# Kernel optimization log

Measured on AMD Instinct MI355X. Metric: run time of the kernel, lower is better.

Reference implementation:

```python
import jax, jax.numpy as jnp
import numpy as np
import math

N = 16384          # batch
F = 39             # field_size = len(feature_sizes)
V = 100000         # vocab per field
E = 16             # embedding_size
D = F * E          # d_model = 624
H = F              # heads = field_size
DK = D // H        # d_k = 16
L = 5              # len(hidden_dims) attention layers
OUT_DIM = 4
NUM_FFW = OUT_DIM * 3


def setup_inputs() -> dict:
    key = jax.random.key(0)
    ks = jax.random.split(key, 24)
    Xi = jax.random.randint(ks[0], (N, F, 1), 0, V, dtype=jnp.int64)
    Xv = jax.random.uniform(ks[1], (N, F), dtype=jnp.float32)
    # embedding tables (stacked across fields; all fields share vocab size)
    emb1 = jax.random.normal(ks[2], (F, V, 1), dtype=jnp.float32) * 0.02
    emb2 = jax.random.normal(ks[3], (F, V, E), dtype=jnp.float32) * 0.02
    # attention layer params, stacked over L layers; torch Linear stored as (in, out)
    s = 1.0 / math.sqrt(D)
    Wq = jax.random.normal(ks[4], (L, D, D), dtype=jnp.float32) * s
    Wk = jax.random.normal(ks[5], (L, D, D), dtype=jnp.float32) * s
    Wv = jax.random.normal(ks[6], (L, D, D), dtype=jnp.float32) * s
    Wo = jax.random.normal(ks[7], (L, D, D), dtype=jnp.float32) * s
    bq = jnp.zeros((L, D), dtype=jnp.float32)
    bk = jnp.zeros((L, D), dtype=jnp.float32)
    bv = jnp.zeros((L, D), dtype=jnp.float32)
    bo = jnp.zeros((L, D), dtype=jnp.float32)
    # merge linears: (F->4), (E->4), (D->4)
    m1_w = jax.random.normal(ks[8], (F, OUT_DIM), dtype=jnp.float32) / math.sqrt(F)
    m1_b = jnp.zeros((OUT_DIM,), dtype=jnp.float32)
    m2_w = jax.random.normal(ks[9], (E, OUT_DIM), dtype=jnp.float32) / math.sqrt(E)
    m2_b = jnp.zeros((OUT_DIM,), dtype=jnp.float32)
    m3_w = jax.random.normal(ks[10], (D, OUT_DIM), dtype=jnp.float32) / math.sqrt(D)
    m3_b = jnp.zeros((OUT_DIM,), dtype=jnp.float32)
    ffw_w = jax.random.normal(ks[11], (NUM_FFW, NUM_FFW), dtype=jnp.float32) / math.sqrt(NUM_FFW)
    ffw_b = jnp.zeros((NUM_FFW,), dtype=jnp.float32)
    # fm_dense_linear weight init'd to 1.0 in init_weight()
    fd_w = jnp.ones((NUM_FFW, 2), dtype=jnp.float32)
    fd_b = jnp.zeros((2,), dtype=jnp.float32)
    return dict(Xi=Xi, Xv=Xv, emb1=emb1, emb2=emb2,
                Wq=Wq, bq=bq, Wk=Wk, bk=bk, Wv=Wv, bv=bv, Wo=Wo, bo=bo,
                m1_w=m1_w, m1_b=m1_b, m2_w=m2_w, m2_b=m2_b, m3_w=m3_w, m3_b=m3_b,
                ffw_w=ffw_w, ffw_b=ffw_b, fd_w=fd_w, fd_b=fd_b)


def reference(Xi, Xv, emb1, emb2, Wq, bq, Wk, bk, Wv, bv, Wo, bo,
              m1_w, m1_b, m2_w, m2_b, m3_w, m3_b, ffw_w, ffw_b, fd_w, fd_b):
    idx = Xi[:, :, 0]                       # (N, F)
    far = jnp.arange(F)[None, :]            # (1, F) field index
    # --- FM first order: gather 1-d embeddings, scale by Xv ---
    f1 = emb1[far, idx][..., 0] * Xv        # (N, F)
    # --- FM second order: gather E-dim embeddings, scale, L2-normalize over fields ---
    xv = emb2[far, idx] * Xv[:, :, None]    # (N, F, E)
    norm = jnp.maximum(jnp.linalg.norm(xv, axis=1, keepdims=True), 1e-12)
    xv = xv / norm
    s1 = jnp.sum(xv, axis=1) ** 2           # (N, E)
    s2 = jnp.sum(xv ** 2, axis=1)           # (N, E)
    f2 = 0.5 * (s1 - s2)                    # (N, E)
    # --- deep part: stacked seq-len-1 multi-head attention ---
    x = xv.reshape(xv.shape[0], D)          # (N, D) deep_emb; deep_k = deep_q = x
    out = x
    inv_sqrt_dk = 1.0 / math.sqrt(DK)
    for l in range(L):
        # call is att(deep_k, deep_q, deep_out) -> forward(q=deep_k, k=deep_q, v=deep_out)
        q = (x @ Wq[l] + bq[l]).reshape(-1, H, DK)
        k = (x @ Wk[l] + bk[l]).reshape(-1, H, DK)
        v = (out @ Wv[l] + bv[l]).reshape(-1, H, DK)
        scores = jnp.sum(q * k, axis=-1, keepdims=True) * inv_sqrt_dk  # (N, H, 1)
        att = scores * v                                               # (N, H, DK)
        out = att.reshape(-1, D) @ Wo[l] + bo[l]
    # --- merge + head ---
    h1 = f1 @ m1_w + m1_b                   # (N, 4)
    h2 = f2 @ m2_w + m2_b                   # (N, 4)
    h3 = out @ m3_w + m3_b                  # (N, 4)
    ffw_in = jnp.concatenate([h1, h2, h3], axis=1)   # (N, 12)
    ffw_out = jax.nn.relu(ffw_in @ ffw_w + ffw_b)    # (N, 12); dropout off (overfitting=True)
    total = ffw_out @ fd_w + fd_b                    # (N, 2)
    return total
```

## Files before the change

kernel.cpp:

```cpp
#include <hip/hip_runtime.h>
#include <cstdint>
#include <cstddef>

typedef __bf16 bf16;
typedef __bf16 bf16x8 __attribute__((ext_vector_type(8)));
typedef float f32x4 __attribute__((ext_vector_type(4)));

#define GLD_LDS16(gp, lp)                                                              \
  __builtin_amdgcn_global_load_lds((const __attribute__((address_space(1))) void*)(gp), \
                                   (__attribute__((address_space(3))) void*)(lp), 16, 0, 0)

namespace {
constexpr int kN  = 16384;
constexpr int kF  = 39;
constexpr int kV  = 100000;
constexpr int kE  = 16;
constexpr int kD  = 624;
constexpr int kDP = 640;
constexpr int kL  = 5;
}

__global__ void wconv_kernel(const float* __restrict__ Wq, const float* __restrict__ Wk,
                             const float* __restrict__ Wv, const float* __restrict__ Wo,
                             bf16* __restrict__ wt) {
  const int mi  = blockIdx.y;
  const int typ = mi / 5, lay = mi % 5;
  const float* W = (typ == 0 ? Wq : typ == 1 ? Wk : typ == 2 ? Wv : Wo) + (size_t)lay * kD * kD;
  bf16* dst = wt + (size_t)mi * kDP * kDP;
  const int bj = blockIdx.x % 20;
  const int bk = blockIdx.x / 20;
  __shared__ float tl[32][33];
  const int tx = threadIdx.x & 31, ty = threadIdx.x >> 5;
#pragma unroll
  for (int i = 0; i < 4; ++i) {
    const int k = bk * 32 + ty + i * 8;
    const int j = bj * 32 + tx;
    tl[ty + i * 8][tx] = (k < kD && j < kD) ? W[k * kD + j] : 0.f;
  }
  __syncthreads();
#pragma unroll
  for (int i = 0; i < 4; ++i) {
    const int j = bj * 32 + ty + i * 8;
    const int k = bk * 32 + tx;
    dst[j * kDP + k] = (bf16)tl[tx][ty + i * 8];
  }
}

__global__ void embed_kernel(const int* __restrict__ Xi, const float* __restrict__ Xv,
                             const float* __restrict__ emb1, const float* __restrict__ emb2,
                             bf16* __restrict__ xb, float* __restrict__ f1, float* __restrict__ f2) {
  const int wid = threadIdx.x >> 6, lane = threadIdx.x & 63;
  const int n = blockIdx.x * 4 + wid;
  __shared__ float xv_s[4][kF][kE];
  __shared__ float inv_s[4][kE];
  const int g = lane >> 4, e = lane & 15;
#pragma unroll
  for (int fb = 0; fb < 10; ++fb) {
    const int f = fb * 4 + g;
    if (f < kF) {
      const int idx   = Xi[n * kF + f];
      const float sc  = Xv[n * kF + f];
      const float v   = emb2[(f * kV + idx) * kE + e] * sc;
      xv_s[wid][f][e] = v;
      if (e == 0) f1[n * 40 + f] = emb1[f * kV + idx] * sc;
    }
  }
  __syncthreads();
  if (lane < kE) {
    float s = 0.f, s2 = 0.f;
    for (int f = 0; f < kF; ++f) { const float v = xv_s[wid][f][lane]; s += v; s2 += v * v; }
    const float nrm = fmaxf(sqrtf(s2), 1e-12f);
    const float inv = 1.f / nrm;
    inv_s[wid][lane] = inv;
    const float s1 = s * inv;
    f2[n * kE + lane] = 0.5f * (s1 * s1 - s2 * inv * inv);
  }
  __syncthreads();
  const float inv = inv_s[wid][e];
#pragma unroll
  for (int fb = 0; fb < 10; ++fb) {
    const int f = fb * 4 + g;
    if (f < kF) xb[(size_t)n * kDP + f * kE + e] = (bf16)(xv_s[wid][f][e] * inv);
  }
  if (lane < 16) xb[(size_t)n * kDP + kD + lane] = (bf16)0.f;
}

template <int MODE>
__global__ __launch_bounds__(256) void gemm_kernel(const bf16* __restrict__ A,
                                                   const bf16* __restrict__ Bt,
                                                   const float* __restrict__ bias,
                                                   const float* __restrict__ scr,
                                                   bf16* __restrict__ Dst) {
  __shared__ bf16 As[128 * 32];
  __shared__ bf16 Bs[128 * 32];
  const int lane = threadIdx.x & 63;
  const int wid  = threadIdx.x >> 6;
  const int wm = wid >> 1, wn = wid & 1;
  const int row0 = blockIdx.x * 128;
  const int col0 = blockIdx.y * 128;

  f32x4 acc[4][4] = {};

  const int lr  = lane >> 2;
  const int sl  = lane & 3;
  const int lsl = sl ^ ((lr >> 1) & 3);
  const size_t aoff0 = (size_t)(row0 + wid * 32 +      lr) * kDP + lsl * 8;
  const size_t aoff1 = (size_t)(row0 + wid * 32 + 16 + lr) * kDP + lsl * 8;
  const size_t boff0 = (size_t)(col0 + wid * 32 +      lr) * kDP + lsl * 8;
  const size_t boff1 = (size_t)(col0 + wid * 32 + 16 + lr) * kDP + lsl * 8;
  bf16* asd0 = As + wid * 1024;
  bf16* asd1 = As + wid * 1024 + 512;
  bf16* bsd0 = Bs + wid * 1024;
  bf16* bsd1 = Bs + wid * 1024 + 512;

  const int rsel = lane & 15;
  const int roff = ((lane >> 4) ^ ((rsel >> 1) & 3)) * 8;

  for (int kt = 0; kt < kDP / 32; ++kt) {
    const int k0 = kt * 32;
    GLD_LDS16(A  + aoff0 + k0, asd0);
    GLD_LDS16(A  + aoff1 + k0, asd1);
    GLD_LDS16(Bt + boff0 + k0, bsd0);
    GLD_LDS16(Bt + boff1 + k0, bsd1);
    __syncthreads();
    bf16x8 av[4], bvv[4];
#pragma unroll
    for (int m = 0; m < 4; ++m)
      av[m] = *(const bf16x8*)(As + (wm * 64 + m * 16 + rsel) * 32 + roff);
#pragma unroll
    for (int nn = 0; nn < 4; ++nn)
      bvv[nn] = *(const bf16x8*)(Bs + (wn * 64 + nn * 16 + rsel) * 32 + roff);
#pragma unroll
    for (int m = 0; m < 4; ++m)
#pragma unroll
      for (int nn = 0; nn < 4; ++nn)
        acc[m][nn] = __builtin_amdgcn_mfma_f32_16x16x32_bf16(av[m], bvv[nn], acc[m][nn], 0, 0, 0);
    __syncthreads();
  }

  const int crow = (lane >> 4) * 4;
  const int ccol = lane & 15;
#pragma unroll
  for (int m = 0; m < 4; ++m) {
#pragma unroll
    for (int nn = 0; nn < 4; ++nn) {
      const int gcol = col0 + wn * 64 + nn * 16 + ccol;
      const float bb = (gcol < kD) ? bias[gcol] : 0.f;
#pragma unroll
      for (int r = 0; r < 4; ++r) {
        const int grow = row0 + wm * 64 + m * 16 + crow + r;
        float v = acc[m][nn][r] + bb;
        if (MODE == 1) v *= (gcol < kD) ? scr[grow * 40 + (gcol >> 4)] : 0.f;
        Dst[(size_t)grow * kDP + gcol] = (bf16)v;
      }
    }
  }
}

__global__ void scores_kernel(const bf16* __restrict__ q, const bf16* __restrict__ k,
                              float* __restrict__ s) {
  const int t = blockIdx.x * 256 + threadIdx.x;
  const int n = t / kF;
  const int h = t - n * kF;
  const bf16x8* qp = (const bf16x8*)(q + (size_t)n * kDP + h * 16);
  const bf16x8* kp = (const bf16x8*)(k + (size_t)n * kDP + h * 16);
  const bf16x8 q0 = qp[0], q1 = qp[1];
  const bf16x8 k0 = kp[0], k1 = kp[1];
  float acc = 0.f;
#pragma unroll
  for (int i = 0; i < 8; ++i) acc += (float)q0[i] * (float)k0[i] + (float)q1[i] * (float)k1[i];
  s[n * 40 + h] = acc * 0.25f;
}

__global__ void head_kernel(const bf16* __restrict__ outb, const float* __restrict__ f1,
                            const float* __restrict__ f2,
                            const float* __restrict__ m1w, const float* __restrict__ m1b,
                            const float* __restrict__ m2w, const float* __restrict__ m2b,
                            const float* __restrict__ m3w, const float* __restrict__ m3b,
                            const float* __restrict__ fww, const float* __restrict__ fwb,
                            const float* __restrict__ fdw, const float* __restrict__ fdb,
                            float* __restrict__ out) {
  const int wid = threadIdx.x >> 6, lane = threadIdx.x & 63;
  const int n = blockIdx.x * 4 + wid;
  float acc[12];
#pragma unroll
  for (int i = 0; i < 12; ++i) acc[i] = 0.f;
  for (int d = lane; d < kD; d += 64) {
    const float v = (float)outb[(size_t)n * kDP + d];
#pragma unroll
    for (int c = 0; c < 4; ++c) acc[8 + c] += v * m3w[d * 4 + c];
  }
  if (lane < kF) {
    const float v = f1[n * 40 + lane];
#pragma unroll
    for (int c = 0; c < 4; ++c) acc[c] += v * m1w[lane * 4 + c];
  }
  if (lane < kE) {
    const float v = f2[n * kE + lane];
#pragma unroll
    for (int c = 0; c < 4; ++c) acc[4 + c] += v * m2w[lane * 4 + c];
  }
#pragma unroll
  for (int off = 32; off > 0; off >>= 1) {
#pragma unroll
    for (int i = 0; i < 12; ++i) acc[i] += __shfl_down(acc[i], off);
  }
  if (lane == 0) {
    float in[12];
#pragma unroll
    for (int c = 0; c < 4; ++c) {
      in[c]     = acc[c]     + m1b[c];
      in[4 + c] = acc[4 + c] + m2b[c];
      in[8 + c] = acc[8 + c] + m3b[c];
    }
    float o0 = fdb[0], o1 = fdb[1];
#pragma unroll
    for (int j = 0; j < 12; ++j) {
      float h = fwb[j];
#pragma unroll
      for (int i = 0; i < 12; ++i) h += in[i] * fww[i * 12 + j];
      h = fmaxf(h, 0.f);
      o0 += h * fdw[j * 2 + 0];
      o1 += h * fdw[j * 2 + 1];
    }
    out[n * 2 + 0] = o0;
    out[n * 2 + 1] = o1;
  }
}

extern "C" void kernel_launch(void* const* d_in, const int* in_sizes, int n_in,
                              void* d_out, int out_size, void* d_ws, size_t ws_size,
                              hipStream_t stream) {
  (void)in_sizes; (void)n_in; (void)out_size; (void)ws_size;
  const int*   Xi   = (const int*)d_in[0];
  const float* Xv   = (const float*)d_in[1];
  const float* emb1 = (const float*)d_in[2];
  const float* emb2 = (const float*)d_in[3];
  const float* Wq   = (const float*)d_in[4];
  const float* bq   = (const float*)d_in[5];
  const float* Wk   = (const float*)d_in[6];
  const float* bk   = (const float*)d_in[7];
  const float* Wv   = (const float*)d_in[8];
  const float* bv   = (const float*)d_in[9];
  const float* Wo   = (const float*)d_in[10];
  const float* bo   = (const float*)d_in[11];
  const float* m1w  = (const float*)d_in[12];
  const float* m1b  = (const float*)d_in[13];
  const float* m2w  = (const float*)d_in[14];
  const float* m2b  = (const float*)d_in[15];
  const float* m3w  = (const float*)d_in[16];
  const float* m3b  = (const float*)d_in[17];
  const float* fww  = (const float*)d_in[18];
  const float* fwb  = (const float*)d_in[19];
  const float* fdw  = (const float*)d_in[20];
  const float* fdb  = (const float*)d_in[21];

  char* p = (char*)d_ws;
  auto carve = [&](size_t bytes) { char* r = p; p += (bytes + 255) & ~(size_t)255; return r; };
  bf16*  wt   = (bf16*)carve((size_t)20 * kDP * kDP * sizeof(bf16));
  bf16*  xb   = (bf16*)carve((size_t)kN * kDP * sizeof(bf16));
  bf16*  outb = (bf16*)carve((size_t)kN * kDP * sizeof(bf16));
  bf16*  qb   = (bf16*)carve((size_t)kN * kDP * sizeof(bf16));
  bf16*  kbuf = (bf16*)carve((size_t)kN * kDP * sizeof(bf16));
  float* scr  = (float*)carve((size_t)kN * 40 * sizeof(float));
  float* f1b  = (float*)carve((size_t)kN * 40 * sizeof(float));
  float* f2b  = (float*)carve((size_t)kN * kE * sizeof(float));

  wconv_kernel<<<dim3(400, 20), 256, 0, stream>>>(Wq, Wk, Wv, Wo, wt);
  embed_kernel<<<kN / 4, 256, 0, stream>>>(Xi, Xv, emb1, emb2, xb, f1b, f2b);

  const dim3 ggrid(kN / 128, kDP / 128);
  const size_t wsz = (size_t)kDP * kDP;
  for (int l = 0; l < kL; ++l) {
    gemm_kernel<0><<<ggrid, 256, 0, stream>>>(xb, wt + (size_t)(0 * 5 + l) * wsz, bq + l * kD, nullptr, qb);
    gemm_kernel<0><<<ggrid, 256, 0, stream>>>(xb, wt + (size_t)(1 * 5 + l) * wsz, bk + l * kD, nullptr, kbuf);
    scores_kernel<<<kN * kF / 256, 256, 0, stream>>>(qb, kbuf, scr);
    gemm_kernel<1><<<ggrid, 256, 0, stream>>>(l == 0 ? xb : outb, wt + (size_t)(2 * 5 + l) * wsz,
                                              bv + l * kD, scr, qb);
    gemm_kernel<0><<<ggrid, 256, 0, stream>>>(qb, wt + (size_t)(3 * 5 + l) * wsz, bo + l * kD, nullptr, outb);
  }
  head_kernel<<<kN / 4, 256, 0, stream>>>(outb, f1b, f2b, m1w, m1b, m2w, m2b, m3w, m3b,
                                          fww, fwb, fdw, fdb, (float*)d_out);
}
```

Baseline: 963.1 us.

## Batch all Q/K projections into one wide GEMM and double GEMM K-tile

Q and K depend only on the input embedding, so the weights for all five layers are interleaved into one 6400-column matrix and computed by a single large GEMM, followed by one scores launch covering every layer. This replaces ten small GEMM launches and five scores launches with two, improving GPU fill and reuse of the A tiles. The GEMM K-tile grows from 32 to 64 with an 8-way LDS swizzle, halving the barrier count per tile at the cost of more shared memory. A padded bias buffer is built so the epilogue can drop its bounds check, and the design needs a large extra workspace holding Q and K for all layers (about 200 MB).

```diff
diff --git a/kernel.cpp b/kernel.cpp
--- a/kernel.cpp
+++ b/kernel.cpp
@@ -18,14 +18,17 @@
 constexpr int kD  = 624;
 constexpr int kDP = 640;
 constexpr int kL  = 5;
+constexpr int kQK = 6400;
 }
 
 __global__ void wconv_kernel(const float* __restrict__ Wq, const float* __restrict__ Wk,
                              const float* __restrict__ Wv, const float* __restrict__ Wo,
                              bf16* __restrict__ wt) {
-  const int mi  = blockIdx.y;
-  const int typ = mi / 5, lay = mi % 5;
-  const float* W = (typ == 0 ? Wq : typ == 1 ? Wk : typ == 2 ? Wv : Wo) + (size_t)lay * kD * kD;
+  const int mi = blockIdx.y;
+  const float* W;
+  if (mi < 10)      W = ((mi & 1) ? Wk : Wq) + (size_t)(mi >> 1) * kD * kD;
+  else if (mi < 15) W = Wv + (size_t)(mi - 10) * kD * kD;
+  else              W = Wo + (size_t)(mi - 15) * kD * kD;
   bf16* dst = wt + (size_t)mi * kDP * kDP;
   const int bj = blockIdx.x % 20;
   const int bk = blockIdx.x / 20;
@@ -43,6 +46,23 @@
     const int j = bj * 32 + ty + i * 8;
     const int k = bk * 32 + tx;
     dst[j * kDP + k] = (bf16)tl[tx][ty + i * 8];
+  }
+}
+
+__global__ void biasbuild_kernel(const float* __restrict__ bq, const float* __restrict__ bk,
+                                 const float* __restrict__ bv, const float* __restrict__ bo,
+                                 float* __restrict__ biasqk, float* __restrict__ biasv,
+                                 float* __restrict__ biaso) {
+  const int idx = blockIdx.x * 256 + threadIdx.x;
+  if (idx < 6400) {
+    const int l = idx / 1280, t = (idx % 1280) / 640, c = idx % 640;
+    biasqk[idx] = (c < kD) ? (t ? bk : bq)[l * kD + c] : 0.f;
+  } else if (idx < 9600) {
+    const int j = idx - 6400, l = j / 640, c = j % 640;
+    biasv[j] = (c < kD) ? bv[l * kD + c] : 0.f;
+  } else {
+    const int j = idx - 9600, l = j / 640, c = j % 640;
+    biaso[j] = (c < kD) ? bo[l * kD + c] : 0.f;
   }
 }
 
@@ -85,14 +105,14 @@
   if (lane < 16) xb[(size_t)n * kDP + kD + lane] = (bf16)0.f;
 }
 
-template <int MODE>
+template <int MODE, int DSTRIDE>
 __global__ __launch_bounds__(256) void gemm_kernel(const bf16* __restrict__ A,
                                                    const bf16* __restrict__ Bt,
                                                    const float* __restrict__ bias,
                                                    const float* __restrict__ scr,
                                                    bf16* __restrict__ Dst) {
-  __shared__ bf16 As[128 * 32];
-  __shared__ bf16 Bs[128 * 32];
+  __shared__ bf16 As[128 * 64];
+  __shared__ bf16 Bs[128 * 64];
   const int lane = threadIdx.x & 63;
   const int wid  = threadIdx.x >> 6;
   const int wm = wid >> 1, wn = wid & 1;
@@ -101,75 +121,81 @@
 
   f32x4 acc[4][4] = {};
 
-  const int lr  = lane >> 2;
-  const int sl  = lane & 3;
-  const int lsl = sl ^ ((lr >> 1) & 3);
-  const size_t aoff0 = (size_t)(row0 + wid * 32 +      lr) * kDP + lsl * 8;
-  const size_t aoff1 = (size_t)(row0 + wid * 32 + 16 + lr) * kDP + lsl * 8;
-  const size_t boff0 = (size_t)(col0 + wid * 32 +      lr) * kDP + lsl * 8;
-  const size_t boff1 = (size_t)(col0 + wid * 32 + 16 + lr) * kDP + lsl * 8;
-  bf16* asd0 = As + wid * 1024;
-  bf16* asd1 = As + wid * 1024 + 512;
-  bf16* bsd0 = Bs + wid * 1024;
-  bf16* bsd1 = Bs + wid * 1024 + 512;
+  const int lr  = lane >> 3;
+  const int sl  = lane & 7;
+  const int lsl = sl ^ lr;
+  size_t aoff[4], boff[4];
+#pragma unroll
+  for (int r = 0; r < 4; ++r) {
+    const int c = wid * 4 + r;
+    aoff[r] = (size_t)(row0 + c * 8 + lr) * kDP + lsl * 8;
+    boff[r] = (size_t)(col0 + c * 8 + lr) * kDP + lsl * 8;
+  }
 
   const int rsel = lane & 15;
-  const int roff = ((lane >> 4) ^ ((rsel >> 1) & 3)) * 8;
-
-  for (int kt = 0; kt < kDP / 32; ++kt) {
-    const int k0 = kt * 32;
-    GLD_LDS16(A  + aoff0 + k0, asd0);
-    GLD_LDS16(A  + aoff1 + k0, asd1);
-    GLD_LDS16(Bt + boff0 + k0, bsd0);
-    GLD_LDS16(Bt + boff1 + k0, bsd1);
+  const int hi   = lane >> 4;
+  const int swz  = rsel & 7;
+
+  for (int kt = 0; kt < kDP / 64; ++kt) {
+    const int k0 = kt * 64;
+#pragma unroll
+    for (int r = 0; r < 4; ++r) {
+      GLD_LDS16(A  + aoff[r] + k0, As + (wid * 4 + r) * 512);
+      GLD_LDS16(Bt + boff[r] + k0, Bs + (wid * 4 + r) * 512);
+    }
     __syncthreads();
-    bf16x8 av[4], bvv[4];
-#pragma unroll
-    for (int m = 0; m < 4; ++m)
-      av[m] = *(const bf16x8*)(As + (wm * 64 + m * 16 + rsel) * 32 + roff);
-#pragma unroll
-    for (int nn = 0; nn < 4; ++nn)
-      bvv[nn] = *(const bf16x8*)(Bs + (wn * 64 + nn * 16 + rsel) * 32 + roff);
-#pragma unroll
-    for (int m = 0; m < 4; ++m)
+#pragma unroll
+    for (int kk = 0; kk < 2; ++kk) {
+      const int ro = ((kk * 4 + hi) ^ swz) * 8;
+      bf16x8 av[4], bvv[4];
+#pragma unroll
+      for (int m = 0; m < 4; ++m)
+        av[m] = *(const bf16x8*)(As + (wm * 64 + m * 16 + rsel) * 64 + ro);
 #pragma unroll
       for (int nn = 0; nn < 4; ++nn)
-        acc[m][nn] = __builtin_amdgcn_mfma_f32_16x16x32_bf16(av[m], bvv[nn], acc[m][nn], 0, 0, 0);
+        bvv[nn] = *(const bf16x8*)(Bs + (wn * 64 + nn * 16 + rsel) * 64 + ro);
+#pragma unroll
+      for (int m = 0; m < 4; ++m)
+#pragma unroll
+        for (int nn = 0; nn < 4; ++nn)
+          acc[m][nn] = __builtin_amdgcn_mfma_f32_16x16x32_bf16(av[m], bvv[nn], acc[m][nn], 0, 0, 0);
+    }
     __syncthreads();
   }
 
-  const int crow = (lane >> 4) * 4;
-  const int ccol = lane & 15;
+  const int crow = hi * 4;
+  const int ccol = rsel;
 #pragma unroll
   for (int m = 0; m < 4; ++m) {
 #pragma unroll
     for (int nn = 0; nn < 4; ++nn) {
       const int gcol = col0 + wn * 64 + nn * 16 + ccol;
-      const float bb = (gcol < kD) ? bias[gcol] : 0.f;
+      const float bb = bias[gcol];
 #pragma unroll
       for (int r = 0; r < 4; ++r) {
         const int grow = row0 + wm * 64 + m * 16 + crow + r;
         float v = acc[m][nn][r] + bb;
         if (MODE == 1) v *= (gcol < kD) ? scr[grow * 40 + (gcol >> 4)] : 0.f;
-        Dst[(size_t)grow * kDP + gcol] = (bf16)v;
+        Dst[(size_t)grow * DSTRIDE + gcol] = (bf16)v;
       }
     }
   }
 }
 
-__global__ void scores_kernel(const bf16* __restrict__ q, const bf16* __restrict__ k,
-                              float* __restrict__ s) {
-  const int t = blockIdx.x * 256 + threadIdx.x;
-  const int n = t / kF;
-  const int h = t - n * kF;
-  const bf16x8* qp = (const bf16x8*)(q + (size_t)n * kDP + h * 16);
-  const bf16x8* kp = (const bf16x8*)(k + (size_t)n * kDP + h * 16);
+__global__ void scores_kernel(const bf16* __restrict__ qk, float* __restrict__ scr) {
+  const int idx = blockIdx.x * 256 + threadIdx.x;
+  const int l   = idx / (kN * kF);
+  const int rem = idx % (kN * kF);
+  const int n   = rem / kF;
+  const int h   = rem % kF;
+  const bf16x8* qp = (const bf16x8*)(qk + (size_t)n * kQK + l * 1280 + h * 16);
+  const bf16x8* kp = (const bf16x8*)(qk + (size_t)n * kQK + l * 1280 + 640 + h * 16);
   const bf16x8 q0 = qp[0], q1 = qp[1];
   const bf16x8 k0 = kp[0], k1 = kp[1];
   float acc = 0.f;
 #pragma unroll
   for (int i = 0; i < 8; ++i) acc += (float)q0[i] * (float)k0[i] + (float)q1[i] * (float)k1[i];
-  s[n * 40 + h] = acc * 0.25f;
+  scr[((size_t)l * kN + n) * 40 + h] = acc * 0.25f;
 }
 
 __global__ void head_kernel(const bf16* __restrict__ outb, const float* __restrict__ f1,
@@ -257,27 +283,32 @@
 
   char* p = (char*)d_ws;
   auto carve = [&](size_t bytes) { char* r = p; p += (bytes + 255) & ~(size_t)255; return r; };
-  bf16*  wt   = (bf16*)carve((size_t)20 * kDP * kDP * sizeof(bf16));
-  bf16*  xb   = (bf16*)carve((size_t)kN * kDP * sizeof(bf16));
-  bf16*  outb = (bf16*)carve((size_t)kN * kDP * sizeof(bf16));
-  bf16*  qb   = (bf16*)carve((size_t)kN * kDP * sizeof(bf16));
-  bf16*  kbuf = (bf16*)carve((size_t)kN * kDP * sizeof(bf16));
-  float* scr  = (float*)carve((size_t)kN * 40 * sizeof(float));
-  float* f1b  = (float*)carve((size_t)kN * 40 * sizeof(float));
-  float* f2b  = (float*)carve((size_t)kN * kE * sizeof(float));
+  bf16*  wt     = (bf16*)carve((size_t)20 * kDP * kDP * sizeof(bf16));
+  bf16*  xb     = (bf16*)carve((size_t)kN * kDP * sizeof(bf16));
+  bf16*  outb   = (bf16*)carve((size_t)kN * kDP * sizeof(bf16));
+  bf16*  attb   = (bf16*)carve((size_t)kN * kDP * sizeof(bf16));
+  bf16*  qk     = (bf16*)carve((size_t)kN * kQK * sizeof(bf16));
+  float* scrA   = (float*)carve((size_t)kL * kN * 40 * sizeof(float));
+  float* f1b    = (float*)carve((size_t)kN * 40 * sizeof(float));
+  float* f2b    = (float*)carve((size_t)kN * kE * sizeof(float));
+  float* biasqk = (float*)carve((size_t)kQK * sizeof(float));
+  float* biasv  = (float*)carve((size_t)kL * kDP * sizeof(float));
+  float* biaso  = (float*)carve((size_t)kL * kDP * sizeof(float));
 
   wconv_kernel<<<dim3(400, 20), 256, 0, stream>>>(Wq, Wk, Wv, Wo, wt);
+  biasbuild_kernel<<<50, 256, 0, stream>>>(bq, bk, bv, bo, biasqk, biasv, biaso);
   embed_kernel<<<kN / 4, 256, 0, stream>>>(Xi, Xv, emb1, emb2, xb, f1b, f2b);
 
+  const size_t wsz = (size_t)kDP * kDP;
+  gemm_kernel<0, kQK><<<dim3(kN / 128, kQK / 128), 256, 0, stream>>>(xb, wt, biasqk, nullptr, qk);
+  scores_kernel<<<kL * kN * kF / 256, 256, 0, stream>>>(qk, scrA);
+
   const dim3 ggrid(kN / 128, kDP / 128);
-  const size_t wsz = (size_t)kDP * kDP;
   for (int l = 0; l < kL; ++l) {
-    gemm_kernel<0><<<ggrid, 256, 0, stream>>>(xb, wt + (size_t)(0 * 5 + l) * wsz, bq + l * kD, nullptr, qb);
-    gemm_kernel<0><<<ggrid, 256, 0, stream>>>(xb, wt + (size_t)(1 * 5 + l) * wsz, bk + l * kD, nullptr, kbuf);
-    scores_kernel<<<kN * kF / 256, 256, 0, stream>>>(qb, kbuf, scr);
-    gemm_kernel<1><<<ggrid, 256, 0, stream>>>(l == 0 ? xb : outb, wt + (size_t)(2 * 5 + l) * wsz,
-                                              bv + l * kD, scr, qb);
-    gemm_kernel<0><<<ggrid, 256, 0, stream>>>(qb, wt + (size_t)(3 * 5 + l) * wsz, bo + l * kD, nullptr, outb);
+    gemm_kernel<1, kDP><<<ggrid, 256, 0, stream>>>(l == 0 ? xb : outb, wt + (size_t)(10 + l) * wsz,
+                                                   biasv + l * kDP, scrA + (size_t)l * kN * 40, attb);
+    gemm_kernel<0, kDP><<<ggrid, 256, 0, stream>>>(attb, wt + (size_t)(15 + l) * wsz,
+                                                   biaso + l * kDP, nullptr, outb);
   }
   head_kernel<<<kN / 4, 256, 0, stream>>>(outb, f1b, f2b, m1w, m1b, m2w, m2b, m3w, m3b,
                                           fww, fwb, fdw, fdb, (float*)d_out);
```

Measured after the change: 1.145 ms. +18.9%, slower.
